# Kernel optimization log

Hardware: AMD Instinct MI355X
Metric: run time of the kernel (lower is better)

The kernel has to match this reference:

```python
import jax, jax.numpy as jnp
import numpy as np

# LLRDenoiser config (init_kwargs): ndim=2, patch W=8, stride S=4, ths=0.1, rand_shift=False
P = 8      # patch size (isotropic)
STRIDE = 4 # patch stride
THS = 0.1  # soft-threshold on singular values
B, C, H, W = 2, 16, 512, 512  # batch, coefficient axis, spatial dims


def setup_inputs() -> dict:
    key = jax.random.key(0)
    x = jax.random.normal(key, (B, C, H, W), dtype=jnp.float32)
    return {"x": x}


def _patch_idx(n, p, s):
    # start indices for sliding windows, inclusive of last full window
    starts = jnp.arange(0, n - p + 1, s)
    return starts[:, None] + jnp.arange(p)[None, :]  # (n_patches, p)


def _llr_denoise(x):
    idx_h = _patch_idx(H, P, STRIDE)  # (nH, P)
    idx_w = _patch_idx(W, P, STRIDE)  # (nW, P)
    nH, nW = idx_h.shape[0], idx_w.shape[0]
    hi = idx_h[:, None, :, None]  # (nH, 1, P, 1)
    wi = idx_w[None, :, None, :]  # (1, nW, 1, P)

    # extract overlapping patches -> (B, C, nH, nW, P, P)
    patches = x[:, :, hi, wi]
    # Casorati matrices per patch: (B, nH*nW, C, P*P)
    mats = patches.transpose(0, 2, 3, 1, 4, 5).reshape(B, nH * nW, C, P * P)

    # batched thin SVD + soft-threshold of singular values
    u, s, vh = jnp.linalg.svd(mats, full_matrices=False)
    s_st = jnp.sign(s) * jnp.maximum(jnp.abs(s) - THS, 0.0)
    mats = (u * s_st[..., None, :]) @ vh

    # back to patch layout (B, C, nH, nW, P, P)
    patches = mats.reshape(B, nH, nW, C, P, P).transpose(0, 3, 1, 2, 4, 5)

    # overlap-add reconstruction, averaged by patch coverage count
    out = jnp.zeros_like(x).at[:, :, hi, wi].add(patches)
    cnt = jnp.zeros((H, W), x.dtype).at[hi[..., 0, :, :] if False else idx_h[:, None, :, None], idx_w[None, :, None, :]].add(1.0)
    return out / cnt


def reference(x):
    return _llr_denoise(x)
```

## Files before the change

### kernel.cpp

```cpp
#include <hip/hip_runtime.h>


#define NBATCH  2
#define NCH     16
#define HDIM    512
#define WDIM    512
#define NPH     127
#define NPW     127
#define NPATCH  (NBATCH * NPH * NPW)
#define NCELL   128
#define THS     0.1f
#define NSIT    8

typedef short bf16x8 __attribute__((ext_vector_type(8)));
typedef float f32x4  __attribute__((ext_vector_type(4)));

#define MFMA(a,b,c) __builtin_amdgcn_mfma_f32_16x16x32_bf16((a),(b),(c),0,0,0)

static __device__ inline short f2bf(float x) {
  return __builtin_bit_cast(short, (__bf16)x);
}
static __device__ inline float blo2f(unsigned int v) {
  return __builtin_bit_cast(float, v << 16);
}
static __device__ inline float bhi2f(unsigned int v) {
  return __builtin_bit_cast(float, v & 0xffff0000u);
}
static __device__ inline unsigned int pack2bf(float lo, float hi) {
  unsigned int a = (unsigned short)f2bf(lo);
  unsigned int b = (unsigned short)f2bf(hi);
  return (b << 16) | a;
}

static __device__ inline int xcd_swz(int b, int nwg) {
  const int q = nwg >> 3, r = nwg & 7;
  const int x = b & 7, lo = b >> 3;
  return (x < r ? x * (q + 1) : r * (q + 1) + (x - r) * q) + lo;
}

static __device__ inline bf16x8 fragc(f32x4 v) {
  bf16x8 r;
  r[0] = f2bf(v[0]); r[1] = f2bf(v[1]); r[2] = f2bf(v[2]); r[3] = f2bf(v[3]);
  r[4] = 0; r[5] = 0; r[6] = 0; r[7] = 0;
  return r;
}

#define ZS_NBLK ((NPATCH + 3) / 4)
__global__ __launch_bounds__(256) void llr_zs(const float* __restrict__ x,
                                              uint2* __restrict__ zs) {
  const int blk = xcd_swz(blockIdx.x, ZS_NBLK);
  const int pid = blk * 4 + (threadIdx.x >> 6);
  if (pid >= NPATCH) return;
  const int bi  = pid / (NPH * NPW);
  const int pr  = pid % (NPH * NPW);
  const int ph  = pr / NPW, pw = pr % NPW;
  const int h0  = ph * 4, w0 = pw * 4;
  const int l   = threadIdx.x & 63;
  const int j   = l & 15;
  const int u   = l >> 4;

  const size_t HW = (size_t)HDIM * WDIM;
  const float* xb = x + (size_t)bi * NCH * HW;

  const float* pb = xb + (size_t)j * HW + (size_t)h0 * WDIM + w0;
  const int dh0 = (u >> 1), dw0 = 4 * (u & 1);
  float4 q0 = *(const float4*)(pb + (size_t)(dh0 + 0) * WDIM + dw0);
  float4 q1 = *(const float4*)(pb + (size_t)(dh0 + 2) * WDIM + dw0);
  float4 q2 = *(const float4*)(pb + (size_t)(dh0 + 4) * WDIM + dw0);
  float4 q3 = *(const float4*)(pb + (size_t)(dh0 + 6) * WDIM + dw0);

  bf16x8 m0, m1;
  m0[0]=f2bf(q0.x); m0[1]=f2bf(q0.y); m0[2]=f2bf(q0.z); m0[3]=f2bf(q0.w);
  m0[4]=f2bf(q1.x); m0[5]=f2bf(q1.y); m0[6]=f2bf(q1.z); m0[7]=f2bf(q1.w);
  m1[0]=f2bf(q2.x); m1[1]=f2bf(q2.y); m1[2]=f2bf(q2.z); m1[3]=f2bf(q2.w);
  m1[4]=f2bf(q3.x); m1[5]=f2bf(q3.y); m1[6]=f2bf(q3.z); m1[7]=f2bf(q3.w);

  f32x4 g = {0.f, 0.f, 0.f, 0.f};
  g = MFMA(m0, m0, g);
  g = MFMA(m1, m1, g);

  float s2 = g[0]*g[0] + g[1]*g[1] + g[2]*g[2] + g[3]*g[3];
  #pragma unroll
  for (int m = 32; m >= 1; m >>= 1) s2 += __shfl_xor(s2, m, 64);

  uint2 wv = {0u, 0u};
  if (s2 > 1e-20f) {
    const float invf  = rsqrtf(s2);
    const float gsc   = 2.0f * invf;
    const float alpha = THS * sqrtf(gsc);

    f32x4 Yc, Zc;
    #pragma unroll
    for (int r = 0; r < 4; ++r) {
      Yc[r] = g[r] * gsc;
      Zc[r] = (4 * u + r == j) ? 1.0f : 0.0f;
    }

    const f32x4 zero = {0.f, 0.f, 0.f, 0.f};
    for (int it = 0; it < NSIT - 1; ++it) {
      bf16x8 yF = fragc(Yc), zF = fragc(Zc);
      f32x4 t  = MFMA(zF, yF, zero);
      bf16x8 tF = fragc(t);
      f32x4 py = MFMA(yF, tF, zero);
      f32x4 pz = MFMA(tF, zF, zero);
      #pragma unroll
      for (int r = 0; r < 4; ++r) {
        Yc[r] = 1.5f * Yc[r] - 0.5f * py[r];
        Zc[r] = 1.5f * Zc[r] - 0.5f * pz[r];
      }
    }
    {
      bf16x8 yF = fragc(Yc), zF = fragc(Zc);
      f32x4 t  = MFMA(zF, yF, zero);
      bf16x8 tF = fragc(t);
      f32x4 pz = MFMA(tF, zF, zero);
      #pragma unroll
      for (int r = 0; r < 4; ++r) Zc[r] = 1.5f * Zc[r] - 0.5f * pz[r];
    }

    wv.x = pack2bf(alpha * Zc[0], alpha * Zc[1]);
    wv.y = pack2bf(alpha * Zc[2], alpha * Zc[3]);
  }
  zs[(size_t)pid * 64 + l] = wv;
}

#define ST_SEG  4
#define ST_NBLK (NBATCH * NCELL * ST_SEG)

#define XLOADS(OFF)                                              \
  _Pragma("unroll")                                              \
  for (int m = 0; m < 16; ++m) {                                 \
    const int e = (m + (OFF)) & 15;                              \
    xv[e] = *(const float2*)(px + (size_t)e * HW);               \
  }

__global__ __launch_bounds__(256, 4) void llr_strip(const float* __restrict__ x,
                                                    const uint2* __restrict__ zs,
                                                    float* __restrict__ out) {
  __shared__ unsigned int Wl[32 * 128];

  const int bid = blockIdx.x;
  const int seg = bid & 3;
  const int ci  = (bid >> 2) & 127;
  const int bi  = bid >> 9;
  const int t   = threadIdx.x;
  const int r   = t >> 6;
  const int q2  = t & 63;

  const size_t HW = (size_t)HDIM * WDIM;
  const float* xb = x + (size_t)bi * NCH * HW;
  float* ob = out + (size_t)bi * NCH * HW;

  const int h   = 4 * ci + r;
  const int wpx = seg * 128 + 2 * q2;
  const float* px = xb + (size_t)h * WDIM + wpx;
  float2 xv[16];
  switch ((bid + r) & 3) {
    case 0: XLOADS(0)  break;
    case 1: XLOADS(4)  break;
    case 2: XLOADS(8)  break;
    default: XLOADS(12) break;
  }

  {
    const int l = t & 63;
    const int u = l >> 4, j = l & 15;
    const float cnth = 2.0f - (ci == 0) - (ci == NCELL - 1);
    const uint2* zb = zs + (size_t)bi * NPH * NPW * 64;
    const int ph0 = (ci > 0) ? ci - 1 : 0;
    const int ph1 = (ci < NPH) ? ci : NPH - 1;
    const bool vh0 = (ci > 0), vh1 = (ci < NPH);

    #pragma unroll
    for (int half = 0; half < 2; ++half) {
      uint2 zv[4][4];
      int   cja[4];
      #pragma unroll
      for (int i = 0; i < 4; ++i) {
        const int c  = (half * 4 + i) * 4 + r;
        const int cj = seg * 32 + c;
        cja[i] = cj;
        const int pw0 = (cj > 0) ? cj - 1 : 0;
        const int pw1 = (cj < NPW) ? cj : NPW - 1;
        zv[i][0] = zb[((size_t)ph0 * NPW + pw0) * 64 + l];
        zv[i][1] = zb[((size_t)ph0 * NPW + pw1) * 64 + l];
        zv[i][2] = zb[((size_t)ph1 * NPW + pw0) * 64 + l];
        zv[i][3] = zb[((size_t)ph1 * NPW + pw1) * 64 + l];
      }
      #pragma unroll
      for (int i = 0; i < 4; ++i) {
        const int c  = (half * 4 + i) * 4 + r;
        const int cj = cja[i];
        const bool vw0 = (cj > 0), vw1 = (cj < NPW);
        float a0 = 0.f, a1 = 0.f, a2 = 0.f, a3 = 0.f;
        #pragma unroll
        for (int k = 0; k < 4; ++k) {
          const bool ok = (k < 2 ? vh0 : vh1) && ((k & 1) == 0 ? vw0 : vw1);
          uint2 z = zv[i][k];
          if (!ok) { z.x = 0u; z.y = 0u; }
          a0 += blo2f(z.x); a1 += bhi2f(z.x);
          a2 += blo2f(z.y); a3 += bhi2f(z.y);
        }
        const float cntw = 2.0f - (cj == 0) - (cj == NCELL - 1);
        const float s = 1.0f / (cnth * cntw);
        const int base = c * 128;
        const int u0 = 8 * u + (j >> 2);
        const int u1 = u0 + 4;
        Wl[base + (((u0 + c) & 31) << 2) + (j & 3)] = pack2bf(s * a0, s * a1);
        Wl[base + (((u1 + c) & 31) << 2) + (j & 3)] = pack2bf(s * a2, s * a3);
      }
    }
  }
  __syncthreads();

  const int cl = q2 >> 1;
  float* po = ob + (size_t)h * WDIM + wpx;
  #pragma unroll
  for (int cp = 0; cp < 8; ++cp) {
    float2 d0 = {0.f, 0.f};
    float2 d1 = {0.f, 0.f};
    #pragma unroll
    for (int k = 0; k < 4; ++k) {
      const uint4 V = *(const uint4*)&Wl[cl * 128 + (((4 * cp + k + cl) & 31) << 2)];
      const unsigned int va[4] = {V.x, V.y, V.z, V.w};
      #pragma unroll
      for (int c = 0; c < 4; ++c) {
        const int e = 4 * k + c;
        const float wlo = blo2f(va[c]);
        const float whi = bhi2f(va[c]);
        d0.x += wlo * xv[e].x; d0.y += wlo * xv[e].y;
        d1.x += whi * xv[e].x; d1.y += whi * xv[e].y;
      }
    }
    const int c0 = 2 * cp, c1 = 2 * cp + 1;
    float2 o0, o1;
    o0.x = xv[c0].x - d0.x; o0.y = xv[c0].y - d0.y;
    o1.x = xv[c1].x - d1.x; o1.y = xv[c1].y - d1.y;
    *(float2*)(po + (size_t)c0 * HW) = o0;
    *(float2*)(po + (size_t)c1 * HW) = o1;
  }
}

extern "C" void kernel_launch(void* const* d_in, const int* in_sizes, int n_in,
                              void* d_out, int out_size, void* d_ws, size_t ws_size,
                              hipStream_t stream) {
  const float* x = (const float*)d_in[0];
  float* out = (float*)d_out;
  uint2* zs = (uint2*)d_ws;

  llr_zs<<<dim3(ZS_NBLK), dim3(256), 0, stream>>>(x, zs);
  llr_strip<<<dim3(ST_NBLK), dim3(256), 0, stream>>>(x, zs, out);
}
```

Baseline: 47.52 us.

## Stage strip input and output through LDS to reassign channel-row loads per wave

Each wave now loads and stores four channels across all four rows of the cell strip, instead of all sixteen channels for a single row. The data is transposed through a new 32 KB shared buffer so the compute phase keeps its per-row, all-channel register layout. This is meant to make each wave's global accesses cover fewer distinct channel planes, which should improve DRAM page and channel locality. In exchange it adds LDS traffic, two extra barriers and more shared memory, and the launch-bounds occupancy hint drops from 4 to 3 blocks.

After: 59.38 us. 1.25x slower.

```diff
diff --git a/kernel.cpp b/kernel.cpp
--- a/kernel.cpp
+++ b/kernel.cpp
@@ -126,18 +126,11 @@
 
 #define ST_SEG  4
 #define ST_NBLK (NBATCH * NCELL * ST_SEG)
-
-#define XLOADS(OFF)                                              \
-  _Pragma("unroll")                                              \
-  for (int m = 0; m < 16; ++m) {                                 \
-    const int e = (m + (OFF)) & 15;                              \
-    xv[e] = *(const float2*)(px + (size_t)e * HW);               \
-  }
-
-__global__ __launch_bounds__(256, 4) void llr_strip(const float* __restrict__ x,
+__global__ __launch_bounds__(256, 3) void llr_strip(const float* __restrict__ x,
                                                     const uint2* __restrict__ zs,
                                                     float* __restrict__ out) {
   __shared__ unsigned int Wl[32 * 128];
+  __shared__ float Xf[16 * 4 * 128];
 
   const int bid = blockIdx.x;
   const int seg = bid & 3;
@@ -145,25 +138,23 @@
   const int bi  = bid >> 9;
   const int t   = threadIdx.x;
   const int r   = t >> 6;
-  const int q2  = t & 63;
+  const int l   = t & 63;
 
   const size_t HW = (size_t)HDIM * WDIM;
   const float* xb = x + (size_t)bi * NCH * HW;
   float* ob = out + (size_t)bi * NCH * HW;
-
-  const int h   = 4 * ci + r;
-  const int wpx = seg * 128 + 2 * q2;
-  const float* px = xb + (size_t)h * WDIM + wpx;
-  float2 xv[16];
-  switch ((bid + r) & 3) {
-    case 0: XLOADS(0)  break;
-    case 1: XLOADS(4)  break;
-    case 2: XLOADS(8)  break;
-    default: XLOADS(12) break;
-  }
+  const int wbase = seg * 128;
+  const int h0 = 4 * ci;
+
+  float2 xr[4][4];
+  #pragma unroll
+  for (int rho = 0; rho < 4; ++rho)
+    #pragma unroll
+    for (int i = 0; i < 4; ++i)
+      xr[i][rho] = *(const float2*)(xb + (size_t)(4 * r + i) * HW
+                                       + (size_t)(h0 + rho) * WDIM + wbase + 2 * l);
 
   {
-    const int l = t & 63;
     const int u = l >> 4, j = l & 15;
     const float cnth = 2.0f - (ci == 0) - (ci == NCELL - 1);
     const uint2* zb = zs + (size_t)bi * NPH * NPW * 64;
@@ -211,10 +202,23 @@
       }
     }
   }
+
+  #pragma unroll
+  for (int i = 0; i < 4; ++i)
+    #pragma unroll
+    for (int rho = 0; rho < 4; ++rho)
+      *(float2*)&Xf[((4 * r + i) * 4 + rho) * 128 + 2 * l] = xr[i][rho];
   __syncthreads();
 
+  const int q2 = l;
+  float2 xl[16];
+  #pragma unroll
+  for (int e = 0; e < 16; ++e)
+    xl[e] = *(const float2*)&Xf[(e * 4 + r) * 128 + 2 * q2];
+  __syncthreads();
+
   const int cl = q2 >> 1;
-  float* po = ob + (size_t)h * WDIM + wpx;
+  float2 ov[16];
   #pragma unroll
   for (int cp = 0; cp < 8; ++cp) {
     float2 d0 = {0.f, 0.f};
@@ -228,17 +232,28 @@
         const int e = 4 * k + c;
         const float wlo = blo2f(va[c]);
         const float whi = bhi2f(va[c]);
-        d0.x += wlo * xv[e].x; d0.y += wlo * xv[e].y;
-        d1.x += whi * xv[e].x; d1.y += whi * xv[e].y;
+        d0.x += wlo * xl[e].x; d0.y += wlo * xl[e].y;
+        d1.x += whi * xl[e].x; d1.y += whi * xl[e].y;
       }
     }
     const int c0 = 2 * cp, c1 = 2 * cp + 1;
-    float2 o0, o1;
-    o0.x = xv[c0].x - d0.x; o0.y = xv[c0].y - d0.y;
-    o1.x = xv[c1].x - d1.x; o1.y = xv[c1].y - d1.y;
-    *(float2*)(po + (size_t)c0 * HW) = o0;
-    *(float2*)(po + (size_t)c1 * HW) = o1;
+    ov[c0].x = xl[c0].x - d0.x; ov[c0].y = xl[c0].y - d0.y;
+    ov[c1].x = xl[c1].x - d1.x; ov[c1].y = xl[c1].y - d1.y;
   }
+
+  #pragma unroll
+  for (int e = 0; e < 16; ++e)
+    *(float2*)&Xf[(e * 4 + r) * 128 + 2 * q2] = ov[e];
+  __syncthreads();
+
+  #pragma unroll
+  for (int i = 0; i < 4; ++i)
+    #pragma unroll
+    for (int rho = 0; rho < 4; ++rho) {
+      float2 v = *(const float2*)&Xf[((4 * r + i) * 4 + rho) * 128 + 2 * l];
+      *(float2*)(ob + (size_t)(4 * r + i) * HW
+                    + (size_t)(h0 + rho) * WDIM + wbase + 2 * l) = v;
+    }
 }
 
 extern "C" void kernel_launch(void* const* d_in, const int* in_sizes, int n_in,
```
